# Kernel tuning notes

Hardware: AMD Instinct MI355X
Metric: run time of the kernel (lower is better)

The kernel has to match this reference:

```python
import jax, jax.numpy as jnp
import numpy as np

N_POLAR = 1024
K_TARGET = 512
CRC_DEG = 11
K_POLAR = K_TARGET + CRC_DEG
BS = 65536


def _crc11_matrix(k):
    # CRC11 (5G uplink, k>19): g(x) = x^11 + x^10 + x^9 + x^5 + 1, zero-init register.
    poly = np.array([1, 1, 1, 0, 0, 0, 1, 0, 0, 0, 0, 1], dtype=np.int64)
    G = np.zeros((k, CRC_DEG), dtype=np.int64)
    for i in range(k):
        msg = np.zeros(k + CRC_DEG, dtype=np.int64)
        msg[i] = 1
        for j in range(k):
            if msg[j]:
                msg[j:j + CRC_DEG + 1] ^= poly
        G[i] = msg[k:]
    return G.astype(np.float32)


def _info_pos(n, k_polar):
    # Polarization-weight (beta-expansion) reliability design [Bioglio_Design]:
    # w(i) = sum_j b_j(i) * 2^(0.25*j); info set = k_polar most reliable indices.
    nb = int(np.log2(n))
    idx = np.arange(n)
    bits = (idx[:, None] >> np.arange(nb)[None, :]) & 1
    w = (bits * (2.0 ** (0.25 * np.arange(nb)))[None, :]).sum(axis=1)
    info = np.sort(np.argsort(w)[-k_polar:])
    return info.astype(np.int32)


def _ind_gather(n):
    # Stage-wise butterfly gather indices; pad slot n points to the zero column.
    nb = int(np.log2(n))
    g = np.full((nb, n + 1), n, dtype=np.int32)
    for s in range(nb):
        r = np.arange(n // 2)
        dest = r * 2 - np.mod(r, 2 ** s)
        g[s, dest] = dest + 2 ** s
    return g


def _subblock_idx(n):
    perm = np.array([0, 1, 2, 4, 3, 5, 6, 7, 8, 16, 9, 17, 10, 18, 11, 19,
                     12, 20, 13, 21, 14, 22, 15, 23, 24, 25, 26, 28, 27, 29, 30, 31])
    ni = np.arange(n)
    i = (32 * ni) // n
    return (perm[i] * (n // 32) + ni % (n // 32)).astype(np.int32)


def _channel_idx(n):
    # Triangular interleaver (Sec 5.4.1.3): fill rows, read columns; as index map.
    t = 0
    while t * (t + 1) // 2 < n:
        t += 1
    v = -np.ones((t, t), dtype=np.int64)
    k = 0
    for i in range(t):
        for j in range(t - i):
            if k < n:
                v[i, j] = k
            k += 1
    src = []
    for j in range(t):
        for i in range(t - j):
            if v[i, j] >= 0:
                src.append(v[i, j])
    return np.asarray(src, dtype=np.int32)


def setup_inputs() -> dict:
    key = jax.random.key(0)
    u = jax.random.randint(key, (BS, K_TARGET), 0, 2).astype(jnp.float32)
    crc_gen = jnp.asarray(_crc11_matrix(K_TARGET))
    info_pos = jnp.asarray(_info_pos(N_POLAR, K_POLAR))
    ind_gather = jnp.asarray(_ind_gather(N_POLAR))
    # E == N: rate matching is identity after sub-block interleave; fuse with
    # the uplink channel interleaver into a single output permutation.
    perm_out = jnp.asarray(_subblock_idx(N_POLAR)[_channel_idx(N_POLAR)])
    return {"u": u, "crc_gen": crc_gen, "info_pos": info_pos,
            "ind_gather": ind_gather, "perm_out": perm_out}


def reference(u, crc_gen, info_pos, ind_gather, perm_out):
    # CRC encode (GF(2)-linear => matmul mod 2), append parity.
    parity = jnp.mod(u @ crc_gen, 2.0)
    bits = jnp.concatenate([u, parity], axis=1)          # [bs, k_polar]
    bs = u.shape[0]
    n = ind_gather.shape[1] - 1
    # Subchannel allocation: scatter info+crc bits into non-frozen positions;
    # extra zero pad column at index n for the butterfly gather.
    x = jnp.zeros((bs, n + 1), u.dtype).at[:, info_pos].set(bits)
    # log2(n) butterfly stages: gather partner then XOR (mod-2 add on bits).
    for s in range(ind_gather.shape[0]):
        x = jnp.mod(x + x[:, ind_gather[s]], 2.0)
    # Sub-block interleave + rate matching (E==N) + channel interleave, fused.
    return x[:, :n][:, perm_out]
```

## Files before the change

### kernel.cpp

```cpp
#include <hip/hip_runtime.h>
#include <stdint.h>

#define NPOLAR 1024
#define KT 512
#define KP 523
#define BLOCK 256
#define PITCH 33

__global__ __launch_bounds__(BLOCK) void polar_enc_kernel(
    const float* __restrict__ u,
    const float* __restrict__ crc_gen,
    const int* __restrict__ info_pos,
    const int* __restrict__ perm_out,
    float* __restrict__ out)
{
    __shared__ uint32_t xl[BLOCK * PITCH];
    __shared__ uint32_t gc[11 * 16];

    const int t   = threadIdx.x;
    const int blk = blockIdx.x;
    const int row = blk * BLOCK + t;

    if (t < 176) {
        int j = t / 16, w = t % 16;
        uint32_t g = 0;
        #pragma unroll
        for (int i = 0; i < 32; ++i) {
            float f = crc_gen[(32 * w + i) * 11 + j];
            g |= ((__float_as_uint(f) >> 29) & 1u) << i;
        }
        gc[j * 16 + w] = g;
    }

    uint32_t uw[16];
    const float4* uv = reinterpret_cast<const float4*>(u + (size_t)row * KT);
    #pragma unroll
    for (int w = 0; w < 16; ++w) {
        uint32_t acc = 0;
        #pragma unroll
        for (int q = 0; q < 8; ++q) {
            float4 f = uv[w * 8 + q];
            acc |= ((__float_as_uint(f.x) >> 29) & 1u) << (4 * q + 0);
            acc |= ((__float_as_uint(f.y) >> 29) & 1u) << (4 * q + 1);
            acc |= ((__float_as_uint(f.z) >> 29) & 1u) << (4 * q + 2);
            acc |= ((__float_as_uint(f.w) >> 29) & 1u) << (4 * q + 3);
        }
        uw[w] = acc;
    }

    __syncthreads();

    uint32_t parity = 0;
    #pragma unroll
    for (int j = 0; j < 11; ++j) {
        uint32_t acc = 0;
        #pragma unroll
        for (int w = 0; w < 16; ++w) acc ^= uw[w] & gc[j * 16 + w];
        parity |= (uint32_t)(__popc(acc) & 1) << j;
    }

    #pragma unroll
    for (int w = 0; w < 32; ++w) xl[t * PITCH + w] = 0;
    {
        int cw = -1; uint32_t cur = 0;
        #pragma unroll
        for (int sw = 0; sw < 17; ++sw) {
            uint32_t src = (sw < 16) ? uw[sw] : parity;
            const int nb = (sw < 16) ? 32 : 11;
            for (int b = 0; b < nb; ++b) {
                int pos = info_pos[sw * 32 + b];
                int w = pos >> 5;
                if (w != cw) {
                    if (cw >= 0) xl[t * PITCH + cw] = cur;
                    cur = 0; cw = w;
                }
                cur |= ((src >> b) & 1u) << (pos & 31);
            }
        }
        xl[t * PITCH + cw] = cur;
    }

    uint32_t x[32];
    #pragma unroll
    for (int w = 0; w < 32; ++w) x[w] = xl[t * PITCH + w];
    #pragma unroll
    for (int w = 0; w < 32; ++w) {
        uint32_t v = x[w];
        v ^= (v >> 1)  & 0x55555555u;
        v ^= (v >> 2)  & 0x33333333u;
        v ^= (v >> 4)  & 0x0F0F0F0Fu;
        v ^= (v >> 8)  & 0x00FF00FFu;
        v ^= (v >> 16) & 0x0000FFFFu;
        x[w] = v;
    }
    #pragma unroll
    for (int d = 1; d <= 16; d <<= 1) {
        #pragma unroll
        for (int w = 0; w < 32; ++w)
            if ((w & d) == 0) x[w] ^= x[w + d];
    }
    #pragma unroll
    for (int w = 0; w < 32; ++w) xl[t * PITCH + w] = x[w];

    __syncthreads();

    const int4 pv = reinterpret_cast<const int4*>(perm_out)[t];
    const int a0 = pv.x >> 5, s0 = pv.x & 31;
    const int a1 = pv.y >> 5, s1 = pv.y & 31;
    const int a2 = pv.z >> 5, s2 = pv.z & 31;
    const int a3 = pv.w >> 5, s3 = pv.w & 31;

    float4* outv = reinterpret_cast<float4*>(out) + (size_t)blk * BLOCK * (NPOLAR / 4) + t;
    #pragma unroll 4
    for (int k = 0; k < BLOCK; ++k) {
        const uint32_t* rowp = &xl[k * PITCH];
        float4 o;
        o.x = (float)((rowp[a0] >> s0) & 1u);
        o.y = (float)((rowp[a1] >> s1) & 1u);
        o.z = (float)((rowp[a2] >> s2) & 1u);
        o.w = (float)((rowp[a3] >> s3) & 1u);
        outv[(size_t)k * (NPOLAR / 4)] = o;
    }
}

extern "C" void kernel_launch(void* const* d_in, const int* in_sizes, int n_in,
                              void* d_out, int out_size, void* d_ws, size_t ws_size,
                              hipStream_t stream) {
    const float* u        = (const float*)d_in[0];
    const float* crc_gen  = (const float*)d_in[1];
    const int*   info_pos = (const int*)d_in[2];
    const int*   perm_out = (const int*)d_in[4];
    float* out = (float*)d_out;

    const int rows = in_sizes[0] / KT;
    const int grid = rows / BLOCK;

    polar_enc_kernel<<<grid, BLOCK, 0, stream>>>(u, crc_gen, info_pos, perm_out, out);
}
```

Measured before the change: 416.5 us.

## Split encoder into pack and expand kernels with coalesced input reads

The single fused kernel is split into two. The first reads u with coalesced float4 loads across threads and packs bits through wave shuffles into shared memory, then runs CRC and the butterfly and writes packed 32-word rows to workspace. The second expands the packed bits through the output permutation, using small 16-row blocks so more blocks are in flight. Info positions are now cached in LDS. This adds a workspace round trip and a second launch, and it falls back to the fused kernel when the workspace is too small.

```diff
diff --git a/kernel.cpp b/kernel.cpp
--- a/kernel.cpp
+++ b/kernel.cpp
@@ -3,11 +3,164 @@
 
 #define NPOLAR 1024
 #define KT 512
-#define KP 523
 #define BLOCK 256
 #define PITCH 33
-
-__global__ __launch_bounds__(BLOCK) void polar_enc_kernel(
+#define PKP 18
+#define ROWS2 16
+
+__device__ __forceinline__ uint32_t fbit(float f) {
+    return (__float_as_uint(f) >> 29) & 1u;
+}
+
+__global__ __launch_bounds__(BLOCK) void polar_pack_kernel(
+    const float* __restrict__ u,
+    const float* __restrict__ crc_gen,
+    const int* __restrict__ info_pos,
+    uint32_t* __restrict__ pko)
+{
+    __shared__ uint32_t pk[BLOCK * PKP];
+    __shared__ uint32_t xl[BLOCK * PITCH];
+    __shared__ uint32_t gc[11 * 16];
+    __shared__ int ip[544];
+
+    const int t   = threadIdx.x;
+    const int blk = blockIdx.x;
+
+    for (int i = t; i < 523; i += BLOCK) ip[i] = info_pos[i];
+
+    if (t < 176) {
+        int j = t / 16, w = t % 16;
+        uint32_t g = 0;
+        #pragma unroll
+        for (int i = 0; i < 32; ++i)
+            g |= fbit(crc_gen[(32 * w + i) * 11 + j]) << i;
+        gc[j * 16 + w] = g;
+    }
+
+    {
+        const int slot = t & 7;
+        const int w0   = (t >> 3) & 15;
+        const int rpar = t >> 7;
+        const float4* uv = reinterpret_cast<const float4*>(u) + (size_t)blk * (BLOCK * KT / 4) + t;
+        #pragma unroll 4
+        for (int i = 0; i < 128; ++i) {
+            float4 f = uv[(size_t)i * 256];
+            uint32_t nib = fbit(f.x) | (fbit(f.y) << 1) | (fbit(f.z) << 2) | (fbit(f.w) << 3);
+            uint32_t val = nib << (slot * 4);
+            val |= __shfl_xor(val, 1);
+            val |= __shfl_xor(val, 2);
+            val |= __shfl_xor(val, 4);
+            if (slot == 0) pk[(rpar + 2 * i) * PKP + w0] = val;
+        }
+    }
+    __syncthreads();
+
+    uint32_t uw[16];
+    #pragma unroll
+    for (int j = 0; j < 8; ++j) {
+        uint2 v = *reinterpret_cast<uint2*>(&pk[t * PKP + 2 * j]);
+        uw[2 * j] = v.x; uw[2 * j + 1] = v.y;
+    }
+    uint32_t parity = 0;
+    #pragma unroll
+    for (int j = 0; j < 11; ++j) {
+        uint32_t acc = 0;
+        #pragma unroll
+        for (int w = 0; w < 16; ++w) acc ^= uw[w] & gc[j * 16 + w];
+        parity |= (uint32_t)(__popc(acc) & 1) << j;
+    }
+
+    #pragma unroll
+    for (int w = 0; w < 32; ++w) xl[t * PITCH + w] = 0;
+    {
+        int cw = -1; uint32_t cur = 0;
+        #pragma unroll
+        for (int sw = 0; sw < 17; ++sw) {
+            uint32_t src = (sw < 16) ? uw[sw] : parity;
+            const int nb = (sw < 16) ? 32 : 11;
+            #pragma unroll 8
+            for (int b = 0; b < nb; ++b) {
+                int pos = ip[sw * 32 + b];
+                int w = pos >> 5;
+                if (w != cw) {
+                    if (cw >= 0) xl[t * PITCH + cw] = cur;
+                    cur = 0; cw = w;
+                }
+                cur |= ((src >> b) & 1u) << (pos & 31);
+            }
+        }
+        xl[t * PITCH + cw] = cur;
+    }
+
+    uint32_t x[32];
+    #pragma unroll
+    for (int w = 0; w < 32; ++w) x[w] = xl[t * PITCH + w];
+    #pragma unroll
+    for (int w = 0; w < 32; ++w) {
+        uint32_t v = x[w];
+        v ^= (v >> 1)  & 0x55555555u;
+        v ^= (v >> 2)  & 0x33333333u;
+        v ^= (v >> 4)  & 0x0F0F0F0Fu;
+        v ^= (v >> 8)  & 0x00FF00FFu;
+        v ^= (v >> 16) & 0x0000FFFFu;
+        x[w] = v;
+    }
+    #pragma unroll
+    for (int d = 1; d <= 16; d <<= 1) {
+        #pragma unroll
+        for (int w = 0; w < 32; ++w)
+            if ((w & d) == 0) x[w] ^= x[w + d];
+    }
+    #pragma unroll
+    for (int w = 0; w < 32; ++w) xl[t * PITCH + w] = x[w];
+    __syncthreads();
+
+    uint32_t* dst = pko + (size_t)blk * (BLOCK * 32);
+    #pragma unroll
+    for (int i = 0; i < 32; ++i) {
+        int f = i * BLOCK + t;
+        dst[f] = xl[(f >> 5) * PITCH + (f & 31)];
+    }
+}
+
+__global__ __launch_bounds__(BLOCK) void polar_expand_kernel(
+    const uint32_t* __restrict__ pki,
+    const int* __restrict__ perm_out,
+    float* __restrict__ out)
+{
+    __shared__ uint32_t xl[ROWS2 * PITCH];
+    const int t   = threadIdx.x;
+    const int blk = blockIdx.x;
+
+    if (t < ROWS2 * 32 / 4) {
+        uint4 v = reinterpret_cast<const uint4*>(pki + (size_t)blk * (ROWS2 * 32))[t];
+        int w4 = t * 4, row = w4 >> 5, w = w4 & 31;
+        xl[row * PITCH + w]     = v.x;
+        xl[row * PITCH + w + 1] = v.y;
+        xl[row * PITCH + w + 2] = v.z;
+        xl[row * PITCH + w + 3] = v.w;
+    }
+    const int4 pv = reinterpret_cast<const int4*>(perm_out)[t];
+    const int a0 = pv.x >> 5, s0 = pv.x & 31;
+    const int a1 = pv.y >> 5, s1 = pv.y & 31;
+    const int a2 = pv.z >> 5, s2 = pv.z & 31;
+    const int a3 = pv.w >> 5, s3 = pv.w & 31;
+    __syncthreads();
+
+    float4* outv = reinterpret_cast<float4*>(out) + (size_t)blk * (ROWS2 * (NPOLAR / 4)) + t;
+    #pragma unroll
+    for (int k = 0; k < ROWS2; ++k) {
+        const uint32_t* rowp = &xl[k * PITCH];
+        float4 o;
+        o.x = (float)((rowp[a0] >> s0) & 1u);
+        o.y = (float)((rowp[a1] >> s1) & 1u);
+        o.z = (float)((rowp[a2] >> s2) & 1u);
+        o.w = (float)((rowp[a3] >> s3) & 1u);
+        outv[(size_t)k * (NPOLAR / 4)] = o;
+    }
+}
+
+__global__ __launch_bounds__(BLOCK) void polar_enc_fused(
     const float* __restrict__ u,
     const float* __restrict__ crc_gen,
     const int* __restrict__ info_pos,
@@ -16,22 +169,15 @@
 {
     __shared__ uint32_t xl[BLOCK * PITCH];
     __shared__ uint32_t gc[11 * 16];
-
-    const int t   = threadIdx.x;
-    const int blk = blockIdx.x;
-    const int row = blk * BLOCK + t;
-
+    const int t = threadIdx.x, blk = blockIdx.x, row = blk * BLOCK + t;
     if (t < 176) {
         int j = t / 16, w = t % 16;
         uint32_t g = 0;
         #pragma unroll
-        for (int i = 0; i < 32; ++i) {
-            float f = crc_gen[(32 * w + i) * 11 + j];
-            g |= ((__float_as_uint(f) >> 29) & 1u) << i;
-        }
+        for (int i = 0; i < 32; ++i)
+            g |= fbit(crc_gen[(32 * w + i) * 11 + j]) << i;
         gc[j * 16 + w] = g;
     }
-
     uint32_t uw[16];
     const float4* uv = reinterpret_cast<const float4*>(u + (size_t)row * KT);
     #pragma unroll
@@ -40,16 +186,12 @@
         #pragma unroll
         for (int q = 0; q < 8; ++q) {
             float4 f = uv[w * 8 + q];
-            acc |= ((__float_as_uint(f.x) >> 29) & 1u) << (4 * q + 0);
-            acc |= ((__float_as_uint(f.y) >> 29) & 1u) << (4 * q + 1);
-            acc |= ((__float_as_uint(f.z) >> 29) & 1u) << (4 * q + 2);
-            acc |= ((__float_as_uint(f.w) >> 29) & 1u) << (4 * q + 3);
+            acc |= fbit(f.x) << (4 * q) | fbit(f.y) << (4 * q + 1)
+                 | fbit(f.z) << (4 * q + 2) | fbit(f.w) << (4 * q + 3);
         }
         uw[w] = acc;
     }
-
-    __syncthreads();
-
+    __syncthreads();
     uint32_t parity = 0;
     #pragma unroll
     for (int j = 0; j < 11; ++j) {
@@ -58,7 +200,6 @@
         for (int w = 0; w < 16; ++w) acc ^= uw[w] & gc[j * 16 + w];
         parity |= (uint32_t)(__popc(acc) & 1) << j;
     }
-
     #pragma unroll
     for (int w = 0; w < 32; ++w) xl[t * PITCH + w] = 0;
     {
@@ -70,46 +211,36 @@
             for (int b = 0; b < nb; ++b) {
                 int pos = info_pos[sw * 32 + b];
                 int w = pos >> 5;
-                if (w != cw) {
-                    if (cw >= 0) xl[t * PITCH + cw] = cur;
-                    cur = 0; cw = w;
-                }
+                if (w != cw) { if (cw >= 0) xl[t * PITCH + cw] = cur; cur = 0; cw = w; }
                 cur |= ((src >> b) & 1u) << (pos & 31);
             }
         }
         xl[t * PITCH + cw] = cur;
     }
-
     uint32_t x[32];
     #pragma unroll
     for (int w = 0; w < 32; ++w) x[w] = xl[t * PITCH + w];
     #pragma unroll
     for (int w = 0; w < 32; ++w) {
         uint32_t v = x[w];
-        v ^= (v >> 1)  & 0x55555555u;
-        v ^= (v >> 2)  & 0x33333333u;
-        v ^= (v >> 4)  & 0x0F0F0F0Fu;
-        v ^= (v >> 8)  & 0x00FF00FFu;
+        v ^= (v >> 1) & 0x55555555u; v ^= (v >> 2) & 0x33333333u;
+        v ^= (v >> 4) & 0x0F0F0F0Fu; v ^= (v >> 8) & 0x00FF00FFu;
         v ^= (v >> 16) & 0x0000FFFFu;
         x[w] = v;
     }
     #pragma unroll
-    for (int d = 1; d <= 16; d <<= 1) {
+    for (int d = 1; d <= 16; d <<= 1)
         #pragma unroll
         for (int w = 0; w < 32; ++w)
             if ((w & d) == 0) x[w] ^= x[w + d];
-    }
     #pragma unroll
     for (int w = 0; w < 32; ++w) xl[t * PITCH + w] = x[w];
-
-    __syncthreads();
-
+    __syncthreads();
     const int4 pv = reinterpret_cast<const int4*>(perm_out)[t];
     const int a0 = pv.x >> 5, s0 = pv.x & 31;
     const int a1 = pv.y >> 5, s1 = pv.y & 31;
     const int a2 = pv.z >> 5, s2 = pv.z & 31;
     const int a3 = pv.w >> 5, s3 = pv.w & 31;
-
     float4* outv = reinterpret_cast<float4*>(out) + (size_t)blk * BLOCK * (NPOLAR / 4) + t;
     #pragma unroll 4
     for (int k = 0; k < BLOCK; ++k) {
@@ -132,8 +263,14 @@
     const int*   perm_out = (const int*)d_in[4];
     float* out = (float*)d_out;
 
-    const int rows = in_sizes[0] / KT;
-    const int grid = rows / BLOCK;
-
-    polar_enc_kernel<<<grid, BLOCK, 0, stream>>>(u, crc_gen, info_pos, perm_out, out);
-}
+    const int rows  = in_sizes[0] / KT;
+    const size_t need = (size_t)rows * 32 * sizeof(uint32_t);
+
+    if (ws_size >= need) {
+        uint32_t* pk = (uint32_t*)d_ws;
+        polar_pack_kernel<<<rows / BLOCK, BLOCK, 0, stream>>>(u, crc_gen, info_pos, pk);
+        polar_expand_kernel<<<rows / ROWS2, BLOCK, 0, stream>>>(pk, perm_out, out);
+    } else {
+        polar_enc_fused<<<rows / BLOCK, BLOCK, 0, stream>>>(u, crc_gen, info_pos, perm_out, out);
+    }
+}
```

Result: slower. 455.4 us (+9.3%).

## Split each codeword across eight threads with coalesced loads and mask-based bit scatter

Applied to the files above, without the earlier changes.

Each codeword row is now handled by eight cooperating threads instead of one, so a block covers 32 rows rather than 256. Input is loaded coalesced, packed into bits with warp shuffles and staged in shared memory. Parity is computed in parallel and combined with shuffles. The per-bit info_pos scatter loop is replaced by a frozen-mask plus prefix-count extraction, and the butterfly stages that span words use shuffles. The aim is to cut the register use, uncoalesced per-row loads and serial scatter of the old version, at the cost of more synchronisation and per-block setup (atomics on the mask, a prefix count) repeated in every one of the now 8x more blocks.

```diff
diff --git a/kernel.cpp b/kernel.cpp
--- a/kernel.cpp
+++ b/kernel.cpp
@@ -3,105 +3,136 @@
 
 #define NPOLAR 1024
 #define KT 512
-#define KP 523
 #define BLOCK 256
-#define PITCH 33
+#define ROWS 32
+#define PKP 18
+#define XLP 36
 
-__global__ __launch_bounds__(BLOCK) void polar_enc_kernel(
+__device__ __forceinline__ uint32_t fbit(float f) {
+    return (__float_as_uint(f) >> 29) & 1u;
+}
+
+__global__ __launch_bounds__(BLOCK, 8) void polar_all_kernel(
     const float* __restrict__ u,
     const float* __restrict__ crc_gen,
     const int* __restrict__ info_pos,
     const int* __restrict__ perm_out,
     float* __restrict__ out)
 {
-    __shared__ uint32_t xl[BLOCK * PITCH];
+    __shared__ uint32_t pk[ROWS * PKP];
+    __shared__ uint32_t xl[ROWS * XLP];
     __shared__ uint32_t gc[11 * 16];
+    __shared__ uint32_t mw[32];
+    __shared__ uint32_t cw[32];
 
     const int t   = threadIdx.x;
     const int blk = blockIdx.x;
-    const int row = blk * BLOCK + t;
+    const int r   = t >> 3;
+    const int q   = t & 7;
 
+    if (t < 32) mw[t] = 0;
+    __syncthreads();
+
+    for (int i = t; i < 523; i += BLOCK) {
+        int pos = info_pos[i];
+        atomicOr(&mw[pos >> 5], 1u << (pos & 31));
+    }
     if (t < 176) {
         int j = t / 16, w = t % 16;
         uint32_t g = 0;
         #pragma unroll
-        for (int i = 0; i < 32; ++i) {
-            float f = crc_gen[(32 * w + i) * 11 + j];
-            g |= ((__float_as_uint(f) >> 29) & 1u) << i;
-        }
+        for (int i = 0; i < 32; ++i)
+            g |= fbit(crc_gen[(32 * w + i) * 11 + j]) << i;
         gc[j * 16 + w] = g;
     }
 
-    uint32_t uw[16];
-    const float4* uv = reinterpret_cast<const float4*>(u + (size_t)row * KT);
-    #pragma unroll
-    for (int w = 0; w < 16; ++w) {
-        uint32_t acc = 0;
+    {
+        const int slot = t & 7;
+        const int w0   = (t >> 3) & 15;
+        const int rpar = t >> 7;
+        const float4* uv = reinterpret_cast<const float4*>(u) + (size_t)blk * (ROWS * KT / 4) + t;
         #pragma unroll
-        for (int q = 0; q < 8; ++q) {
-            float4 f = uv[w * 8 + q];
-            acc |= ((__float_as_uint(f.x) >> 29) & 1u) << (4 * q + 0);
-            acc |= ((__float_as_uint(f.y) >> 29) & 1u) << (4 * q + 1);
-            acc |= ((__float_as_uint(f.z) >> 29) & 1u) << (4 * q + 2);
-            acc |= ((__float_as_uint(f.w) >> 29) & 1u) << (4 * q + 3);
+        for (int i = 0; i < 16; ++i) {
+            float4 f = uv[(size_t)i * 256];
+            uint32_t nib = fbit(f.x) | (fbit(f.y) << 1) | (fbit(f.z) << 2) | (fbit(f.w) << 3);
+            uint32_t val = nib << (slot * 4);
+            val |= __shfl_xor(val, 1);
+            val |= __shfl_xor(val, 2);
+            val |= __shfl_xor(val, 4);
+            if (slot == 0) pk[(rpar + 2 * i) * PKP + w0] = val;
         }
-        uw[w] = acc;
+    }
+    __syncthreads();
+
+    if (t < 32) {
+        uint32_t c = 0;
+        for (int v = 0; v < t; ++v) c += __popc(mw[v]);
+        cw[t] = c;
     }
 
+    {
+        uint32_t a = pk[r * PKP + 2 * q], b = pk[r * PKP + 2 * q + 1];
+        uint32_t par = 0;
+        #pragma unroll
+        for (int j = 0; j < 11; ++j) {
+            uint32_t acc = (a & gc[j * 16 + 2 * q]) ^ (b & gc[j * 16 + 2 * q + 1]);
+            par |= (uint32_t)(__popc(acc) & 1) << j;
+        }
+        par ^= __shfl_xor(par, 1);
+        par ^= __shfl_xor(par, 2);
+        par ^= __shfl_xor(par, 4);
+        if (q == 0) pk[r * PKP + 16] = par;
+        if (q == 1) pk[r * PKP + 17] = 0;
+    }
     __syncthreads();
 
-    uint32_t parity = 0;
-    #pragma unroll
-    for (int j = 0; j < 11; ++j) {
-        uint32_t acc = 0;
+    uint32_t xr[4];
+    {
+        const uint32_t* row = &pk[r * PKP];
         #pragma unroll
-        for (int w = 0; w < 16; ++w) acc ^= uw[w] & gc[j * 16 + w];
-        parity |= (uint32_t)(__popc(acc) & 1) << j;
+        for (int j = 0; j < 4; ++j) {
+            int w = 4 * q + j;
+            uint32_t m = mw[w];
+            uint32_t c = cw[w];
+            int k = c >> 5, sh = c & 31;
+            uint64_t win = (((uint64_t)row[k + 1] << 32) | row[k]) >> sh;
+            uint32_t x;
+            if (m == 0xFFFFFFFFu) {
+                x = (uint32_t)win;
+            } else {
+                x = 0;
+                uint32_t wv = (uint32_t)win;
+                while (m) {
+                    int b = __builtin_ctz(m);
+                    m &= m - 1;
+                    x |= (wv & 1u) << b;
+                    wv >>= 1;
+                }
+            }
+            xr[j] = x;
+        }
     }
 
     #pragma unroll
-    for (int w = 0; w < 32; ++w) xl[t * PITCH + w] = 0;
-    {
-        int cw = -1; uint32_t cur = 0;
-        #pragma unroll
-        for (int sw = 0; sw < 17; ++sw) {
-            uint32_t src = (sw < 16) ? uw[sw] : parity;
-            const int nb = (sw < 16) ? 32 : 11;
-            for (int b = 0; b < nb; ++b) {
-                int pos = info_pos[sw * 32 + b];
-                int w = pos >> 5;
-                if (w != cw) {
-                    if (cw >= 0) xl[t * PITCH + cw] = cur;
-                    cur = 0; cw = w;
-                }
-                cur |= ((src >> b) & 1u) << (pos & 31);
-            }
-        }
-        xl[t * PITCH + cw] = cur;
-    }
-
-    uint32_t x[32];
-    #pragma unroll
-    for (int w = 0; w < 32; ++w) x[w] = xl[t * PITCH + w];
-    #pragma unroll
-    for (int w = 0; w < 32; ++w) {
-        uint32_t v = x[w];
+    for (int j = 0; j < 4; ++j) {
+        uint32_t v = xr[j];
         v ^= (v >> 1)  & 0x55555555u;
         v ^= (v >> 2)  & 0x33333333u;
         v ^= (v >> 4)  & 0x0F0F0F0Fu;
         v ^= (v >> 8)  & 0x00FF00FFu;
         v ^= (v >> 16) & 0x0000FFFFu;
-        x[w] = v;
+        xr[j] = v;
     }
+    xr[0] ^= xr[1]; xr[2] ^= xr[3];
+    xr[0] ^= xr[2]; xr[1] ^= xr[3];
     #pragma unroll
-    for (int d = 1; d <= 16; d <<= 1) {
-        #pragma unroll
-        for (int w = 0; w < 32; ++w)
-            if ((w & d) == 0) x[w] ^= x[w + d];
+    for (int j = 0; j < 4; ++j) {
+        uint32_t p;
+        p = __shfl_xor(xr[j], 1); if ((q & 1) == 0) xr[j] ^= p;
+        p = __shfl_xor(xr[j], 2); if ((q & 2) == 0) xr[j] ^= p;
+        p = __shfl_xor(xr[j], 4); if ((q & 4) == 0) xr[j] ^= p;
     }
-    #pragma unroll
-    for (int w = 0; w < 32; ++w) xl[t * PITCH + w] = x[w];
-
+    *reinterpret_cast<uint4*>(&xl[r * XLP + 4 * q]) = make_uint4(xr[0], xr[1], xr[2], xr[3]);
     __syncthreads();
 
     const int4 pv = reinterpret_cast<const int4*>(perm_out)[t];
@@ -110,10 +141,10 @@
     const int a2 = pv.z >> 5, s2 = pv.z & 31;
     const int a3 = pv.w >> 5, s3 = pv.w & 31;
 
-    float4* outv = reinterpret_cast<float4*>(out) + (size_t)blk * BLOCK * (NPOLAR / 4) + t;
-    #pragma unroll 4
-    for (int k = 0; k < BLOCK; ++k) {
-        const uint32_t* rowp = &xl[k * PITCH];
+    float4* outv = reinterpret_cast<float4*>(out) + (size_t)blk * (ROWS * (NPOLAR / 4)) + t;
+    #pragma unroll
+    for (int k = 0; k < ROWS; ++k) {
+        const uint32_t* rowp = &xl[k * XLP];
         float4 o;
         o.x = (float)((rowp[a0] >> s0) & 1u);
         o.y = (float)((rowp[a1] >> s1) & 1u);
@@ -133,7 +164,7 @@
     float* out = (float*)d_out;
 
     const int rows = in_sizes[0] / KT;
-    const int grid = rows / BLOCK;
+    const int grid = rows / ROWS;
 
-    polar_enc_kernel<<<grid, BLOCK, 0, stream>>>(u, crc_gen, info_pos, perm_out, out);
+    polar_all_kernel<<<grid, BLOCK, 0, stream>>>(u, crc_gen, info_pos, perm_out, out);
 }
```

Result: faster. 383.6 us (-7.9%).
